# Performance work log

Measured on AMD Instinct MI355X. Metric: run time of the kernel, lower is better.

The kernel has to match this reference:

```python
import jax, jax.numpy as jnp
import numpy as np

BATCH = 1_000_000
IN_DIM = 3
OUT_DIM = 64


def setup_inputs() -> dict:
    key = jax.random.key(0)
    ks = jax.random.split(key, 14)
    names = ["S", "X", "Uz", "Ug", "Ur", "Uh", "Wz", "Wg", "Wr", "Wh", "bz", "bg", "br", "bh"]
    shapes = {
        "S": (BATCH, OUT_DIM), "X": (BATCH, IN_DIM),
        "Uz": (IN_DIM, OUT_DIM), "Ug": (IN_DIM, OUT_DIM), "Ur": (IN_DIM, OUT_DIM), "Uh": (IN_DIM, OUT_DIM),
        "Wz": (OUT_DIM, OUT_DIM), "Wg": (OUT_DIM, OUT_DIM), "Wr": (OUT_DIM, OUT_DIM), "Wh": (OUT_DIM, OUT_DIM),
        "bz": (1, OUT_DIM), "bg": (1, OUT_DIM), "br": (1, OUT_DIM), "bh": (1, OUT_DIM),
    }
    scale = {"S": 1.0, "X": 1.0}
    return {n: (jax.random.normal(k, shapes[n], dtype=jnp.float32) * scale.get(n, 0.2))
            for n, k in zip(names, ks)}


def reference(S, X, Uz, Ug, Ur, Uh, Wz, Wg, Wr, Wh, bz, bg, br, bh):
    # Custom DGM LSTM-style gated layer (activation_1 = activation_2 = tanh).
    Z = jnp.tanh(X @ Uz + S @ Wz + bz)
    G = jnp.tanh(X @ Ug + S @ Wg + bg)
    R = jnp.tanh(X @ Ur + S @ Wr + br)
    H = jnp.tanh(X @ Uh + (S * R) @ Wh + bh)
    S_new = (1.0 - G) * H + Z * S
    return S_new
```

## Files before the change

### kernel.cpp

```cpp
#include <hip/hip_runtime.h>

#define NWT   62500
#define GRID  512
#define WPB   4
#define TOTW  (GRID * WPB)

typedef __attribute__((ext_vector_type(8))) short bf16x8;
typedef __attribute__((ext_vector_type(4))) float f32x4;

static __device__ __forceinline__ short f2b(float f) {
    __bf16 h = (__bf16)f;
    return __builtin_bit_cast(short, h);
}
static __device__ __forceinline__ unsigned pack2(float lo, float hi) {
    return ((unsigned)(unsigned short)f2b(lo)) |
           (((unsigned)(unsigned short)f2b(hi)) << 16);
}
static __device__ __forceinline__ float tanh_fast(float x) {
    float e = __expf(2.0f * x);
    return 1.0f - 2.0f * __builtin_amdgcn_rcpf(e + 1.0f);
}

static __device__ __forceinline__ void gate_mm(const bf16x8 (&wR)[2][4],
                                               const char* lBg, const int (&baOff)[4],
                                               bf16x8 aX, bf16x8 a0, bf16x8 a1,
                                               f32x4 (&acc)[4])
{
    #pragma unroll
    for (int nt = 0; nt < 4; ++nt) {
        bf16x8 bx = *(const bf16x8*)(lBg + baOff[nt]);
        f32x4 z4 = {0.f, 0.f, 0.f, 0.f};
        acc[nt] = __builtin_amdgcn_mfma_f32_16x16x32_bf16(bx, aX, z4, 0, 0, 0);
    }
    #pragma unroll
    for (int ks = 0; ks < 2; ++ks) {
        bf16x8 a = ks ? a1 : a0;
        #pragma unroll
        for (int nt = 0; nt < 4; ++nt)
            acc[nt] = __builtin_amdgcn_mfma_f32_16x16x32_bf16(wR[ks][nt], a, acc[nt], 0, 0, 0);
    }
}

__global__ __launch_bounds__(256, 2)
void dgm_lstm_kernel(const float* __restrict__ S, const float* __restrict__ X,
                     const float* __restrict__ U0, const float* __restrict__ U1,
                     const float* __restrict__ U2, const float* __restrict__ U3,
                     const float* __restrict__ W0, const float* __restrict__ W1,
                     const float* __restrict__ W2, const float* __restrict__ W3,
                     const float* __restrict__ b0, const float* __restrict__ b1,
                     const float* __restrict__ b2, const float* __restrict__ b3,
                     float* __restrict__ Out)
{
    __shared__ __align__(16) unsigned short lWT[4][64][64];
    __shared__ __align__(16) unsigned short lBa[4][65][8];
    __shared__ __align__(16) float          lS[WPB][16][68];
    __shared__ __align__(16) unsigned short lR[WPB][16][64];

    const int tid = threadIdx.x;

    {
        const float* Ws[4] = {W0, W1, W2, W3};
        #pragma unroll
        for (int g = 0; g < 4; ++g) {
            #pragma unroll
            for (int it = 0; it < 8; ++it) {
                int p  = it * 256 + tid;
                int n  = p & 63;
                int k2 = (p >> 6) << 1;
                float w0 = Ws[g][k2 * 64 + n];
                float w1 = Ws[g][k2 * 64 + 64 + n];
                int byt = ((n << 7) + (k2 << 1)) ^ ((n & 7) << 4);
                *(unsigned*)((char*)(&lWT[0][0][0]) + (g << 13) + byt) = pack2(w0, w1);
            }
        }
        const float* Us[4] = {U0, U1, U2, U3};
        const float* bs[4] = {b0, b1, b2, b3};
        int g = tid >> 6, n = tid & 63;
        bf16x8 f = {};
        f[0] = f2b(Us[g][n]);       f[1] = f2b(Us[g][64 + n]);
        f[2] = f2b(Us[g][128 + n]); f[3] = f2b(bs[g][n]);
        *(bf16x8*)(&lBa[g][n][0]) = f;
        if (tid < 4) { bf16x8 z = {}; *(bf16x8*)(&lBa[tid][64][0]) = z; }
    }
    __syncthreads();

    const int l   = tid & 63;
    const int wv  = tid >> 6;
    const int l15 = l & 15;
    const int lg  = l >> 4;

    const char* lWb = (const char*)(&lWT[0][0][0]);
    const char* lBb = (const char*)(&lBa[0][0][0]);
    char*       lRw = (char*)(&lR[wv][0][0]);

    bf16x8 wReg[4][2][4];
    #pragma unroll
    for (int g = 0; g < 4; ++g)
        #pragma unroll
        for (int ks = 0; ks < 2; ++ks)
            #pragma unroll
            for (int nt = 0; nt < 4; ++nt) {
                int n = l15 + (nt << 4);
                int byt = ((n << 7) + (ks << 6) + (lg << 4)) ^ ((n & 7) << 4);
                wReg[g][ks][nt] = *(const bf16x8*)(lWb + (g << 13) + byt);
            }

    int baOff[4];
    #pragma unroll
    for (int nt = 0; nt < 4; ++nt)
        baOff[nt] = ((lg == 0) ? (l15 + (nt << 4)) : 64) << 4;
    int wrOff[4];
    #pragma unroll
    for (int nt = 0; nt < 4; ++nt)
        wrOff[nt] = ((l15 << 7) + (nt << 5) + (lg << 3)) ^ ((l15 & 7) << 4);
    int rdOff[2];
    #pragma unroll
    for (int ks = 0; ks < 2; ++ks)
        rdOff[ks] = ((l15 << 7) + (ks << 6) + (lg << 4)) ^ ((l15 & 7) << 4);

    const int gw = blockIdx.x * WPB + wv;
    const short one_bf = (short)0x3F80;

    float4 p0, p1, p2, p3;
    float  px0 = 0.f, px1 = 0.f, px2 = 0.f;
    {
        const float* Sr = S + (size_t)((gw << 4) + l15) * 64 + (lg << 3);
        p0 = *(const float4*)(Sr);      p1 = *(const float4*)(Sr + 4);
        p2 = *(const float4*)(Sr + 32); p3 = *(const float4*)(Sr + 36);
        if (lg == 0) {
            const float* Xr = X + (size_t)((gw << 4) + l15) * 3;
            px0 = Xr[0]; px1 = Xr[1]; px2 = Xr[2];
        }
    }

    for (int wt = gw; wt < NWT; wt += TOTW) {
        const int row0 = wt << 4;

        float* lSr = &lS[wv][l15][0];
        *(float4*)(lSr + (lg << 3))      = p0;
        *(float4*)(lSr + (lg << 3) + 4)  = p1;
        *(float4*)(lSr + (lg << 3) + 32) = p2;
        *(float4*)(lSr + (lg << 3) + 36) = p3;

        bf16x8 aS0, aS1, aX = {};
        aS0[0] = f2b(p0.x); aS0[1] = f2b(p0.y); aS0[2] = f2b(p0.z); aS0[3] = f2b(p0.w);
        aS0[4] = f2b(p1.x); aS0[5] = f2b(p1.y); aS0[6] = f2b(p1.z); aS0[7] = f2b(p1.w);
        aS1[0] = f2b(p2.x); aS1[1] = f2b(p2.y); aS1[2] = f2b(p2.z); aS1[3] = f2b(p2.w);
        aS1[4] = f2b(p3.x); aS1[5] = f2b(p3.y); aS1[6] = f2b(p3.z); aS1[7] = f2b(p3.w);
        aX[0] = f2b(px0); aX[1] = f2b(px1); aX[2] = f2b(px2);
        aX[3] = (lg == 0) ? one_bf : (short)0;

        int tn = wt + TOTW;
        if (tn < NWT) {
            const float* Sr = S + (size_t)((tn << 4) + l15) * 64 + (lg << 3);
            p0 = *(const float4*)(Sr);      p1 = *(const float4*)(Sr + 4);
            p2 = *(const float4*)(Sr + 32); p3 = *(const float4*)(Sr + 36);
            if (lg == 0) {
                const float* Xr = X + (size_t)((tn << 4) + l15) * 3;
                px0 = Xr[0]; px1 = Xr[1]; px2 = Xr[2];
            }
        }

        asm volatile("s_waitcnt lgkmcnt(0)" ::: "memory");
        f32x4 sv[4];
        #pragma unroll
        for (int nt = 0; nt < 4; ++nt)
            sv[nt] = *(const f32x4*)(&lS[wv][l15][(nt << 4) + (lg << 2)]);

        f32x4 acc[4];

        gate_mm(wReg[2], lBb + 2 * 1040, baOff, aX, aS0, aS1, acc);
        #pragma unroll
        for (int nt = 0; nt < 4; ++nt) {
            float sr0 = sv[nt][0] * tanh_fast(acc[nt][0]);
            float sr1 = sv[nt][1] * tanh_fast(acc[nt][1]);
            float sr2 = sv[nt][2] * tanh_fast(acc[nt][2]);
            float sr3 = sv[nt][3] * tanh_fast(acc[nt][3]);
            uint2 w;
            w.x = pack2(sr0, sr1);
            w.y = pack2(sr2, sr3);
            *(uint2*)(lRw + wrOff[nt]) = w;
        }

        f32x4 zs;
        float zsv[4][4];
        gate_mm(wReg[0], lBb, baOff, aX, aS0, aS1, acc);
        #pragma unroll
        for (int nt = 0; nt < 4; ++nt)
            #pragma unroll
            for (int j = 0; j < 4; ++j)
                zsv[nt][j] = tanh_fast(acc[nt][j]) * sv[nt][j];
        (void)zs;

        float gq[4][4];
        gate_mm(wReg[1], lBb + 1040, baOff, aX, aS0, aS1, acc);
        #pragma unroll
        for (int nt = 0; nt < 4; ++nt)
            #pragma unroll
            for (int j = 0; j < 4; ++j)
                gq[nt][j] = 1.0f - tanh_fast(acc[nt][j]);

        asm volatile("s_waitcnt lgkmcnt(0)" ::: "memory");
        bf16x8 aR0 = *(const bf16x8*)(lRw + rdOff[0]);
        bf16x8 aR1 = *(const bf16x8*)(lRw + rdOff[1]);
        gate_mm(wReg[3], lBb + 3 * 1040, baOff, aX, aR0, aR1, acc);

        float* Or = Out + (size_t)(row0 + l15) * 64 + (lg << 2);
        #pragma unroll
        for (int nt = 0; nt < 4; ++nt) {
            float4 o;
            o.x = fmaf(gq[nt][0], tanh_fast(acc[nt][0]), zsv[nt][0]);
            o.y = fmaf(gq[nt][1], tanh_fast(acc[nt][1]), zsv[nt][1]);
            o.z = fmaf(gq[nt][2], tanh_fast(acc[nt][2]), zsv[nt][2]);
            o.w = fmaf(gq[nt][3], tanh_fast(acc[nt][3]), zsv[nt][3]);
            *(float4*)(Or + (nt << 4)) = o;
        }
    }
}

extern "C" void kernel_launch(void* const* d_in, const int* in_sizes, int n_in,
                              void* d_out, int out_size, void* d_ws, size_t ws_size,
                              hipStream_t stream) {
    dim3 grid(GRID), block(256);
    dgm_lstm_kernel<<<grid, block, 0, stream>>>(
        (const float*)d_in[0],  (const float*)d_in[1],
        (const float*)d_in[2],  (const float*)d_in[3],
        (const float*)d_in[4],  (const float*)d_in[5],
        (const float*)d_in[6],  (const float*)d_in[7],
        (const float*)d_in[8],  (const float*)d_in[9],
        (const float*)d_in[10], (const float*)d_in[11],
        (const float*)d_in[12], (const float*)d_in[13],
        (float*)d_out);
}
```

Before: 121.4 us.

## Software-pipeline H gate of previous tile behind R/Z/G gates of next

Splits the loop body so the R, Z and G gates of one tile run in a lambda, and the H gate matmul and output combine for the previous tile run in another. The S*R buffer is double-buffered in LDS so the two stages can interleave. Wh is now read from LDS per use instead of held in registers, and (1-G) is stored packed as bf16 between stages. Together these aim to cut register pressure and give the scheduler independent MFMA and tanh work to overlap. In exchange it adds LDS reads and loses some precision in the G term. tanh also switches to an exp2-based form.

```diff
diff --git a/kernel.cpp b/kernel.cpp
--- a/kernel.cpp
+++ b/kernel.cpp
@@ -16,15 +16,21 @@
     return ((unsigned)(unsigned short)f2b(lo)) |
            (((unsigned)(unsigned short)f2b(hi)) << 16);
 }
+static __device__ __forceinline__ float bflo(unsigned u) {
+    return __builtin_bit_cast(float, u << 16);
+}
+static __device__ __forceinline__ float bfhi(unsigned u) {
+    return __builtin_bit_cast(float, u & 0xffff0000u);
+}
 static __device__ __forceinline__ float tanh_fast(float x) {
-    float e = __expf(2.0f * x);
+    float e = __builtin_exp2f(x * 2.8853900817779268f);
     return 1.0f - 2.0f * __builtin_amdgcn_rcpf(e + 1.0f);
 }
 
-static __device__ __forceinline__ void gate_mm(const bf16x8 (&wR)[2][4],
-                                               const char* lBg, const int (&baOff)[4],
-                                               bf16x8 aX, bf16x8 a0, bf16x8 a1,
-                                               f32x4 (&acc)[4])
+static __device__ __forceinline__ void gate_mm_reg(const bf16x8 (&wR)[2][4],
+                                                   const char* lBg, const int (&baOff)[4],
+                                                   bf16x8 aX, bf16x8 a0, bf16x8 a1,
+                                                   f32x4 (&acc)[4])
 {
     #pragma unroll
     for (int nt = 0; nt < 4; ++nt) {
@@ -54,7 +60,7 @@
     __shared__ __align__(16) unsigned short lWT[4][64][64];
     __shared__ __align__(16) unsigned short lBa[4][65][8];
     __shared__ __align__(16) float          lS[WPB][16][68];
-    __shared__ __align__(16) unsigned short lR[WPB][16][64];
+    __shared__ __align__(16) unsigned short lR[WPB][2][16][64];
 
     const int tid = threadIdx.x;
 
@@ -91,11 +97,11 @@
 
     const char* lWb = (const char*)(&lWT[0][0][0]);
     const char* lBb = (const char*)(&lBa[0][0][0]);
-    char*       lRw = (char*)(&lR[wv][0][0]);
-
-    bf16x8 wReg[4][2][4];
-    #pragma unroll
-    for (int g = 0; g < 4; ++g)
+    char*       lRw = (char*)(&lR[wv][0][0][0]);
+
+    bf16x8 wReg[3][2][4];
+    #pragma unroll
+    for (int g = 0; g < 3; ++g)
         #pragma unroll
         for (int ks = 0; ks < 2; ++ks)
             #pragma unroll
@@ -109,6 +115,14 @@
     #pragma unroll
     for (int nt = 0; nt < 4; ++nt)
         baOff[nt] = ((lg == 0) ? (l15 + (nt << 4)) : 64) << 4;
+    int wOffH[2][4];
+    #pragma unroll
+    for (int ks = 0; ks < 2; ++ks)
+        #pragma unroll
+        for (int nt = 0; nt < 4; ++nt) {
+            int n = l15 + (nt << 4);
+            wOffH[ks][nt] = ((n << 7) + (ks << 6) + (lg << 4)) ^ ((n & 7) << 4);
+        }
     int wrOff[4];
     #pragma unroll
     for (int nt = 0; nt < 4; ++nt)
@@ -133,7 +147,12 @@
         }
     }
 
-    for (int wt = gw; wt < NWT; wt += TOTW) {
+    f32x4  zsC[4];
+    uint2  gqp[4];
+    bf16x8 aXp = {};
+    int    rowH = 0, parH = 0, par = 0;
+
+    auto RZG = [&](int wt) {
         const int row0 = wt << 4;
 
         float* lSr = &lS[wv][l15][0];
@@ -169,7 +188,8 @@
 
         f32x4 acc[4];
 
-        gate_mm(wReg[2], lBb + 2 * 1040, baOff, aX, aS0, aS1, acc);
+        char* lRp = lRw + (par << 11);
+        gate_mm_reg(wReg[2], lBb + 2 * 1040, baOff, aX, aS0, aS1, acc);
         #pragma unroll
         for (int nt = 0; nt < 4; ++nt) {
             float sr0 = sv[nt][0] * tanh_fast(acc[nt][0]);
@@ -179,43 +199,68 @@
             uint2 w;
             w.x = pack2(sr0, sr1);
             w.y = pack2(sr2, sr3);
-            *(uint2*)(lRw + wrOff[nt]) = w;
-        }
-
-        f32x4 zs;
-        float zsv[4][4];
-        gate_mm(wReg[0], lBb, baOff, aX, aS0, aS1, acc);
+            *(uint2*)(lRp + wrOff[nt]) = w;
+        }
+
+        gate_mm_reg(wReg[0], lBb, baOff, aX, aS0, aS1, acc);
         #pragma unroll
         for (int nt = 0; nt < 4; ++nt)
             #pragma unroll
             for (int j = 0; j < 4; ++j)
-                zsv[nt][j] = tanh_fast(acc[nt][j]) * sv[nt][j];
-        (void)zs;
-
-        float gq[4][4];
-        gate_mm(wReg[1], lBb + 1040, baOff, aX, aS0, aS1, acc);
-        #pragma unroll
-        for (int nt = 0; nt < 4; ++nt)
-            #pragma unroll
-            for (int j = 0; j < 4; ++j)
-                gq[nt][j] = 1.0f - tanh_fast(acc[nt][j]);
-
-        asm volatile("s_waitcnt lgkmcnt(0)" ::: "memory");
-        bf16x8 aR0 = *(const bf16x8*)(lRw + rdOff[0]);
-        bf16x8 aR1 = *(const bf16x8*)(lRw + rdOff[1]);
-        gate_mm(wReg[3], lBb + 3 * 1040, baOff, aX, aR0, aR1, acc);
-
-        float* Or = Out + (size_t)(row0 + l15) * 64 + (lg << 2);
+                zsC[nt][j] = tanh_fast(acc[nt][j]) * sv[nt][j];
+
+        gate_mm_reg(wReg[1], lBb + 1040, baOff, aX, aS0, aS1, acc);
+        #pragma unroll
+        for (int nt = 0; nt < 4; ++nt) {
+            float g0 = 1.0f - tanh_fast(acc[nt][0]);
+            float g1 = 1.0f - tanh_fast(acc[nt][1]);
+            float g2 = 1.0f - tanh_fast(acc[nt][2]);
+            float g3 = 1.0f - tanh_fast(acc[nt][3]);
+            gqp[nt].x = pack2(g0, g1);
+            gqp[nt].y = pack2(g2, g3);
+        }
+
+        aXp = aX; rowH = row0; parH = par; par ^= 1;
+    };
+
+    auto HCOMB = [&]() {
+        const char* lRp = lRw + (parH << 11);
+        bf16x8 aR0 = *(const bf16x8*)(lRp + rdOff[0]);
+        bf16x8 aR1 = *(const bf16x8*)(lRp + rdOff[1]);
+        f32x4 acc[4];
+        #pragma unroll
+        for (int nt = 0; nt < 4; ++nt) {
+            bf16x8 bx = *(const bf16x8*)(lBb + 3 * 1040 + baOff[nt]);
+            f32x4 z4 = {0.f, 0.f, 0.f, 0.f};
+            acc[nt] = __builtin_amdgcn_mfma_f32_16x16x32_bf16(bx, aXp, z4, 0, 0, 0);
+        }
+        #pragma unroll
+        for (int ks = 0; ks < 2; ++ks) {
+            bf16x8 a = ks ? aR1 : aR0;
+            #pragma unroll
+            for (int nt = 0; nt < 4; ++nt) {
+                bf16x8 bw = *(const bf16x8*)(lWb + (3 << 13) + wOffH[ks][nt]);
+                acc[nt] = __builtin_amdgcn_mfma_f32_16x16x32_bf16(bw, a, acc[nt], 0, 0, 0);
+            }
+        }
+        float* Or = Out + (size_t)(rowH + l15) * 64 + (lg << 2);
         #pragma unroll
         for (int nt = 0; nt < 4; ++nt) {
             float4 o;
-            o.x = fmaf(gq[nt][0], tanh_fast(acc[nt][0]), zsv[nt][0]);
-            o.y = fmaf(gq[nt][1], tanh_fast(acc[nt][1]), zsv[nt][1]);
-            o.z = fmaf(gq[nt][2], tanh_fast(acc[nt][2]), zsv[nt][2]);
-            o.w = fmaf(gq[nt][3], tanh_fast(acc[nt][3]), zsv[nt][3]);
+            o.x = fmaf(bflo(gqp[nt].x), tanh_fast(acc[nt][0]), zsC[nt][0]);
+            o.y = fmaf(bfhi(gqp[nt].x), tanh_fast(acc[nt][1]), zsC[nt][1]);
+            o.z = fmaf(bflo(gqp[nt].y), tanh_fast(acc[nt][2]), zsC[nt][2]);
+            o.w = fmaf(bfhi(gqp[nt].y), tanh_fast(acc[nt][3]), zsC[nt][3]);
             *(float4*)(Or + (nt << 4)) = o;
         }
-    }
+    };
+
+    RZG(gw);
+    for (int wt = gw + TOTW; wt < NWT; wt += TOTW) {
+        HCOMB();
+        RZG(wt);
+    }
+    HCOMB();
 }
 
 extern "C" void kernel_launch(void* const* d_in, const int* in_sizes, int n_in,
```

New measurement: 139.5 us. +14.9%, slower.
